# Kernel tuning notes

Measured on AMD Instinct MI355X. Metric: run time of the kernel, lower is better.

The kernel has to match this reference:

```python
import jax, jax.numpy as jnp
import numpy as np

N_NODES = 50000
N_EDGES = 800000
HIDDEN = 128
NUM_BASIS = 32
CUTOFF = 5.0


def setup_inputs() -> dict:
    key = jax.random.key(0)
    ks = jax.random.split(key, 9)
    node_features = jax.random.normal(ks[0], (N_NODES, HIDDEN), dtype=jnp.float32)
    positions = jax.random.normal(ks[1], (N_NODES, 3), dtype=jnp.float32)
    edge_index = jax.random.randint(ks[2], (2, N_EDGES), 0, N_NODES)
    edge_in = 2 * HIDDEN + NUM_BASIS
    W1 = jax.random.normal(ks[3], (edge_in, HIDDEN), dtype=jnp.float32) * (edge_in ** -0.5)
    b1 = jnp.zeros((HIDDEN,), dtype=jnp.float32)
    W2 = jax.random.normal(ks[4], (HIDDEN, HIDDEN), dtype=jnp.float32) * (HIDDEN ** -0.5)
    b2 = jnp.zeros((HIDDEN,), dtype=jnp.float32)
    Wo = jax.random.normal(ks[5], (HIDDEN, HIDDEN), dtype=jnp.float32) * (HIDDEN ** -0.5)
    bo = jnp.zeros((HIDDEN,), dtype=jnp.float32)
    return dict(node_features=node_features, positions=positions, edge_index=edge_index,
                W1=W1, b1=b1, W2=W2, b2=b2, Wo=Wo, bo=bo)


def reference(node_features, positions, edge_index, W1, b1, W2, b2, Wo, bo):
    n_nodes = node_features.shape[0]
    # Gaussian radial basis (fixed buffers)
    centers = jnp.linspace(0.0, CUTOFF, NUM_BASIS)  # [NB]
    width = 0.5 * (centers[1] - centers[0] + 0.01)
    src, dst = edge_index[0], edge_index[1]
    rel = positions[dst] - positions[src]                       # [E,3]
    dist = jnp.linalg.norm(rel, axis=-1)                        # [E]
    d = jnp.minimum(dist, CUTOFF)
    rbf = jnp.exp(-0.5 * ((d[:, None] - centers) / width) ** 2)  # [E,NB]
    # edge message: concat(src feats, dst feats, rbf) -> 2-layer SiLU MLP
    msg = jnp.concatenate([node_features[src], node_features[dst], rbf], axis=-1)  # [E,2H+NB]
    h = jax.nn.silu(msg @ W1 + b1) @ W2 + b2                    # [E,H]
    # scatter-add to destination nodes + degree normalization
    updates = jax.ops.segment_sum(h, dst, num_segments=n_nodes)          # [N,H]
    degree = jax.ops.segment_sum(jnp.ones_like(dist), dst, num_segments=n_nodes)
    updates = updates / jnp.maximum(degree, 1.0)[:, None]
    return updates @ Wo + bo
```

## Files before the change

kernel.cpp:

```cpp
#include <hip/hip_runtime.h>
#include <hip/hip_bf16.h>

#define NN 50000
#define NE 800000
#define HID 128
#define NB 32
#define SCAN_B 196

typedef short short8 __attribute__((ext_vector_type(8)));
typedef float f32x4 __attribute__((ext_vector_type(4)));

static __device__ __forceinline__ short f2bf(float x) {
    union { __hip_bfloat16 h; short s; } r;
    r.h = __float2bfloat16(x);
    return r.s;
}
static __device__ __forceinline__ float bf2f(unsigned short s) {
    return __uint_as_float(((unsigned int)s) << 16);
}
static __device__ __forceinline__ unsigned int addpack(unsigned int a, unsigned int b) {
    union { unsigned int u; __hip_bfloat162 h; } x, y, r;
    x.u = a; y.u = b;
    r.h = __hadd2(x.h, y.h);
    return r.u;
}

__global__ void fused_prep(const int* __restrict__ dstI, int* __restrict__ counts,
                           const float* __restrict__ W1, const float* __restrict__ W2,
                           const float* __restrict__ Wo,
                           short* __restrict__ W1aT, short* __restrict__ W1bT,
                           short* __restrict__ W1cT, short* __restrict__ W2t,
                           short* __restrict__ Wot) {
    int b = blockIdx.x;
    if (b < 3125) {
        int e = b * 256 + threadIdx.x;
        atomicAdd(&counts[dstI[e]], 1);
    } else {
        int t = (b - 3125) * 256 + threadIdx.x;
        if (t < 16384) {
            int n = t >> 7, k = t & 127;
            W1aT[t] = f2bf(W1[k * HID + n]);
        } else if ((t -= 16384) < 16384) {
            int n = t >> 7, k = t & 127;
            W1bT[t] = f2bf(W1[(k + 128) * HID + n]);
        } else if ((t -= 16384) < 4096) {
            int n = t >> 5, k = t & 31;
            W1cT[t] = f2bf(W1[(k + 256) * HID + n]);
        } else if ((t -= 4096) < 16384) {
            int n = t >> 7, k = t & 127;
            W2t[t] = f2bf(W2[k * HID + n]);
        } else if ((t -= 16384) < 16384) {
            int n = t >> 7, k = t & 127;
            Wot[t] = f2bf(Wo[k * HID + n]);
        }
    }
}

__global__ void k_scan1(const int* __restrict__ counts, int* __restrict__ scanEx,
                        int* __restrict__ blockSum) {
    __shared__ int s[256];
    int t = threadIdx.x, idx = blockIdx.x * 256 + t;
    int v = counts[idx];
    s[t] = v; __syncthreads();
    #pragma unroll
    for (int off = 1; off < 256; off <<= 1) {
        int x = (t >= off) ? s[t - off] : 0;
        __syncthreads();
        s[t] += x;
        __syncthreads();
    }
    scanEx[idx] = s[t] - v;
    if (t == 255) blockSum[blockIdx.x] = s[255];
}

__global__ void k_scan23(const int* __restrict__ scanEx, const int* __restrict__ blockSum,
                         int* __restrict__ cur) {
    __shared__ int s[256];
    int t = threadIdx.x, b = blockIdx.x;
    s[t] = (t < b) ? blockSum[t] : 0;
    __syncthreads();
    #pragma unroll
    for (int off = 128; off > 0; off >>= 1) {
        if (t < off) s[t] += s[t + off];
        __syncthreads();
    }
    int idx = b * 256 + t;
    cur[idx] = scanEx[idx] + s[0];
}

__global__ void k_permute(const int* __restrict__ src, const int* __restrict__ dst,
                          int* __restrict__ cur, int2* __restrict__ edgeS) {
    int e = blockIdx.x * 256 + threadIdx.x;
    int s = src[e];
    int d = dst[e];
    int r = atomicAdd(&cur[d], 1);
    edgeS[r] = make_int2(s, d);
}

__global__ void sd_kernel(const float* __restrict__ nf,
                          const short* __restrict__ W1aT, const short* __restrict__ W1bT,
                          short* __restrict__ Sg, short* __restrict__ Dg) {
    __shared__ short As[64 * 136];
    const int tid  = threadIdx.x;
    const int wave = tid >> 6;
    const int lane = tid & 63;
    const int quad = lane >> 4;
    const int l15  = lane & 15;
    const int n0   = blockIdx.x * 64;

    {
        int row = tid >> 2, pt = tid & 3;
        int node = min(n0 + row, NN - 1);
        const float4* p = (const float4*)(nf + (size_t)node * HID + pt * 32);
        #pragma unroll
        for (int j = 0; j < 4; ++j) {
            float4 w0 = p[j * 2], w1 = p[j * 2 + 1];
            short8 o;
            o[0] = f2bf(w0.x); o[1] = f2bf(w0.y); o[2] = f2bf(w0.z); o[3] = f2bf(w0.w);
            o[4] = f2bf(w1.x); o[5] = f2bf(w1.y); o[6] = f2bf(w1.z); o[7] = f2bf(w1.w);
            *(short8*)(As + row * 136 + pt * 32 + j * 8) = o;
        }
    }
    __syncthreads();

    f32x4 aS[4][2], aD[4][2];
    #pragma unroll
    for (int mt = 0; mt < 4; ++mt)
        #pragma unroll
        for (int nt = 0; nt < 2; ++nt) {
            aS[mt][nt] = (f32x4){0.f, 0.f, 0.f, 0.f};
            aD[mt][nt] = (f32x4){0.f, 0.f, 0.f, 0.f};
        }

    #pragma unroll
    for (int kk = 0; kk < 4; ++kk) {
        int ko = kk * 32 + quad * 8;
        short8 a[4];
        #pragma unroll
        for (int mt = 0; mt < 4; ++mt)
            a[mt] = *(const short8*)(As + (mt * 16 + l15) * 136 + ko);
        #pragma unroll
        for (int nt = 0; nt < 2; ++nt) {
            int n = wave * 32 + nt * 16 + l15;
            short8 bS = *(const short8*)(W1aT + n * HID + ko);
            short8 bD = *(const short8*)(W1bT + n * HID + ko);
            #pragma unroll
            for (int mt = 0; mt < 4; ++mt) {
                aS[mt][nt] = __builtin_amdgcn_mfma_f32_16x16x32_bf16(a[mt], bS, aS[mt][nt], 0, 0, 0);
                aD[mt][nt] = __builtin_amdgcn_mfma_f32_16x16x32_bf16(a[mt], bD, aD[mt][nt], 0, 0, 0);
            }
        }
    }

    #pragma unroll
    for (int nt = 0; nt < 2; ++nt) {
        int col = wave * 32 + nt * 16 + l15;
        #pragma unroll
        for (int mt = 0; mt < 4; ++mt) {
            #pragma unroll
            for (int r = 0; r < 4; ++r) {
                int node = n0 + mt * 16 + quad * 4 + r;
                if (node < NN) {
                    Sg[(size_t)node * HID + col] = f2bf(aS[mt][nt][r]);
                    Dg[(size_t)node * HID + col] = f2bf(aD[mt][nt][r]);
                }
            }
        }
    }
}

__launch_bounds__(512, 6)
__global__ void edge_kernel(const short* __restrict__ Sg,
                            const short* __restrict__ Dg,
                            const float* __restrict__ pos,
                            const int2* __restrict__ edgeS,
                            const short* __restrict__ W1cT,
                            const float* __restrict__ b1,
                            const short* __restrict__ W2t,
                            const float* __restrict__ b2,
                            float* __restrict__ upd) {
    __shared__ char buf[49152];
    __shared__ int  dn_sh[128];
    short* PRE = (short*)buf;
    short* R   = (short*)(buf + 34816);
    short* Ps  = (short*)buf;
    float* UfT = (float*)buf;

    const int tid  = threadIdx.x;
    const int wave = tid >> 6;
    const int lane = tid & 63;
    const int quad = lane >> 4;
    const int l15  = lane & 15;
    const int mg   = wave >> 2;
    const int nsl  = wave & 3;
    const int e0   = blockIdx.x * 128;

    {
        int es = tid >> 2, pt = tid & 3;
        int2 sd = edgeS[e0 + es];
        int s = sd.x, d = sd.y;
        const int4* sp = (const int4*)(Sg + (size_t)s * HID + pt * 32);
        const int4* dp = (const int4*)(Dg + (size_t)d * HID + pt * 32);
        int4* op = (int4*)(PRE + es * 136 + pt * 32);
        #pragma unroll
        for (int j = 0; j < 4; ++j) {
            int4 a = sp[j], b = dp[j];
            int4 o;
            o.x = addpack(a.x, b.x);
            o.y = addpack(a.y, b.y);
            o.z = addpack(a.z, b.z);
            o.w = addpack(a.w, b.w);
            op[j] = o;
        }
        if (pt == 0) dn_sh[es] = d;
        float dx = pos[d * 3 + 0] - pos[s * 3 + 0];
        float dy = pos[d * 3 + 1] - pos[s * 3 + 1];
        float dz = pos[d * 3 + 2] - pos[s * 3 + 2];
        float dd = fminf(sqrtf(dx * dx + dy * dy + dz * dz), 5.0f);
        const float step  = 5.0f / 31.0f;
        const float width = 0.5f * (step + 0.01f);
        const float coef  = -0.5f / (width * width);
        short8 r;
        #pragma unroll
        for (int j = 0; j < 8; ++j) {
            float c = step * (float)(pt * 8 + j);
            float t = dd - c;
            r[j] = f2bf(__expf(coef * t * t));
        }
        *(short8*)(R + es * 56 + pt * 8) = r;
    }
    __syncthreads();

    f32x4 acc[4][2];
    #pragma unroll
    for (int mt = 0; mt < 4; ++mt)
        #pragma unroll
        for (int nt = 0; nt < 2; ++nt) acc[mt][nt] = (f32x4){0.f, 0.f, 0.f, 0.f};
    {
        int ko = quad * 8;
        short8 a[4];
        #pragma unroll
        for (int mt = 0; mt < 4; ++mt)
            a[mt] = *(const short8*)(R + (mg * 64 + mt * 16 + l15) * 56 + ko);
        #pragma unroll
        for (int nt = 0; nt < 2; ++nt) {
            int n = nsl * 32 + nt * 16 + l15;
            short8 b = *(const short8*)(W1cT + n * NB + ko);
            #pragma unroll
            for (int mt = 0; mt < 4; ++mt)
                acc[mt][nt] = __builtin_amdgcn_mfma_f32_16x16x32_bf16(a[mt], b, acc[mt][nt], 0, 0, 0);
        }
    }

    {
        float b1c[2] = { b1[nsl * 32 + l15], b1[nsl * 32 + 16 + l15] };
        const unsigned short* PREu = (const unsigned short*)PRE;
        #pragma unroll
        for (int nt = 0; nt < 2; ++nt) {
            int col = nsl * 32 + nt * 16 + l15;
            #pragma unroll
            for (int mt = 0; mt < 4; ++mt) {
                #pragma unroll
                for (int r = 0; r < 4; ++r) {
                    int row = mg * 64 + mt * 16 + quad * 4 + r;
                    float pre = bf2f(PREu[row * 136 + col]);
                    float x = acc[mt][nt][r] + pre + b1c[nt];
                    float p = x * __builtin_amdgcn_rcpf(1.0f + __expf(-x));
                    Ps[row * 136 + col] = f2bf(p);
                }
            }
        }
    }
    __syncthreads();

    f32x4 acc2[4][2];
    #pragma unroll
    for (int mt = 0; mt < 4; ++mt)
        #pragma unroll
        for (int nt = 0; nt < 2; ++nt) acc2[mt][nt] = (f32x4){0.f, 0.f, 0.f, 0.f};

    #pragma unroll
    for (int kk = 0; kk < 4; ++kk) {
        int ko = kk * 32 + quad * 8;
        short8 a[4];
        #pragma unroll
        for (int mt = 0; mt < 4; ++mt)
            a[mt] = *(const short8*)(Ps + (mg * 64 + mt * 16 + l15) * 136 + ko);
        #pragma unroll
        for (int nt = 0; nt < 2; ++nt) {
            int n = nsl * 32 + nt * 16 + l15;
            short8 b = *(const short8*)(W2t + n * HID + ko);
            #pragma unroll
            for (int mt = 0; mt < 4; ++mt)
                acc2[mt][nt] = __builtin_amdgcn_mfma_f32_16x16x32_bf16(a[mt], b, acc2[mt][nt], 0, 0, 0);
        }
    }
    __syncthreads();

    float b2c[2] = { b2[nsl * 32 + l15], b2[nsl * 32 + 16 + l15] };
    #pragma unroll
    for (int h = 0; h < 2; ++h) {
        if (mg == h) {
            #pragma unroll
            for (int nt = 0; nt < 2; ++nt) {
                int col = nsl * 32 + nt * 16 + l15;
                #pragma unroll
                for (int mt = 0; mt < 4; ++mt) {
                    f32x4 v;
                    #pragma unroll
                    for (int r = 0; r < 4; ++r) v[r] = acc2[mt][nt][r] + b2c[nt];
                    *(f32x4*)(UfT + col * 68 + mt * 16 + quad * 4) = v;
                }
            }
        }
        __syncthreads();
        {
            int col = tid & 127;
            int seg = tid >> 7;
            int rb  = h * 64 + seg * 16;
            const float* cp = UfT + col * 68 + seg * 16;
            f32x4 vv[4];
            #pragma unroll
            for (int j = 0; j < 4; ++j) vv[j] = *(const f32x4*)(cp + j * 4);
            int rnode = dn_sh[rb];
            float run = 0.0f;
            #pragma unroll
            for (int i = 0; i < 16; ++i) {
                int node = dn_sh[rb + i];
                float v = vv[i >> 2][i & 3];
                if (node != rnode) {
                    atomicAdd(upd + (size_t)rnode * HID + col, run);
                    rnode = node;
                    run = v;
                } else {
                    run += v;
                }
            }
            atomicAdd(upd + (size_t)rnode * HID + col, run);
        }
        __syncthreads();
    }
}

__launch_bounds__(256, 4)
__global__ void out_kernel(float* __restrict__ out,
                           const int* __restrict__ counts,
                           const short* __restrict__ Wot,
                           const float* __restrict__ bo) {
    __shared__ short A2[64 * 136];

    const int tid  = threadIdx.x;
    const int wave = tid >> 6;
    const int lane = tid & 63;
    const int quad = lane >> 4;
    const int l15  = lane & 15;
    const int n0   = blockIdx.x * 64;

    {
        int row = tid >> 2, pt = tid & 3;
        int node = n0 + row;
        if (node < NN) {
            float inv = 1.0f / fmaxf((float)counts[node], 1.0f);
            const float4* p = (const float4*)(out + (size_t)node * HID + pt * 32);
            #pragma unroll
            for (int j = 0; j < 4; ++j) {
                float4 w0 = p[j * 2], w1 = p[j * 2 + 1];
                short8 o;
                o[0] = f2bf(w0.x * inv); o[1] = f2bf(w0.y * inv);
                o[2] = f2bf(w0.z * inv); o[3] = f2bf(w0.w * inv);
                o[4] = f2bf(w1.x * inv); o[5] = f2bf(w1.y * inv);
                o[6] = f2bf(w1.z * inv); o[7] = f2bf(w1.w * inv);
                *(short8*)(A2 + row * 136 + pt * 32 + j * 8) = o;
            }
        } else {
            short8 z = (short8){0, 0, 0, 0, 0, 0, 0, 0};
            #pragma unroll
            for (int j = 0; j < 4; ++j)
                *(short8*)(A2 + row * 136 + pt * 32 + j * 8) = z;
        }
    }
    __syncthreads();

    f32x4 acc[4][2];
    #pragma unroll
    for (int mt = 0; mt < 4; ++mt)
        #pragma unroll
        for (int nt = 0; nt < 2; ++nt) acc[mt][nt] = (f32x4){0.f, 0.f, 0.f, 0.f};

    #pragma unroll
    for (int kk = 0; kk < 4; ++kk) {
        int ko = kk * 32 + quad * 8;
        short8 a[4];
        #pragma unroll
        for (int mt = 0; mt < 4; ++mt)
            a[mt] = *(const short8*)(A2 + (mt * 16 + l15) * 136 + ko);
        #pragma unroll
        for (int nt = 0; nt < 2; ++nt) {
            int n = wave * 32 + nt * 16 + l15;
            short8 b = *(const short8*)(Wot + n * HID + ko);
            #pragma unroll
            for (int mt = 0; mt < 4; ++mt)
                acc[mt][nt] = __builtin_amdgcn_mfma_f32_16x16x32_bf16(a[mt], b, acc[mt][nt], 0, 0, 0);
        }
    }
    __syncthreads();

    #pragma unroll
    for (int nt = 0; nt < 2; ++nt) {
        int col = wave * 32 + nt * 16 + l15;
        float bias = bo[col];
        #pragma unroll
        for (int mt = 0; mt < 4; ++mt) {
            #pragma unroll
            for (int r = 0; r < 4; ++r) {
                int row = mt * 16 + quad * 4 + r;
                int node = n0 + row;
                if (node < NN)
                    out[(size_t)node * HID + col] = acc[mt][nt][r] + bias;
            }
        }
    }
}

extern "C" void kernel_launch(void* const* d_in, const int* in_sizes, int n_in,
                              void* d_out, int out_size, void* d_ws, size_t ws_size,
                              hipStream_t stream) {
    const float* nf  = (const float*)d_in[0];
    const float* pos = (const float*)d_in[1];
    const int*   ei  = (const int*)d_in[2];
    const float* W1  = (const float*)d_in[3];
    const float* b1  = (const float*)d_in[4];
    const float* W2  = (const float*)d_in[5];
    const float* b2  = (const float*)d_in[6];
    const float* Wo  = (const float*)d_in[7];
    const float* bo  = (const float*)d_in[8];
    float* out = (float*)d_out;

    char* ws = (char*)d_ws;
    short* W1aT     = (short*)(ws);
    short* W1bT     = (short*)(ws + 32768);
    short* W1cT     = (short*)(ws + 65536);
    short* W2t      = (short*)(ws + 73728);
    short* Wot      = (short*)(ws + 106496);
    int*   counts   = (int*)(ws + 139264);
    int*   cur      = (int*)(ws + 339968);
    int*   blockSum = (int*)(ws + 540672);
    int2*  edgeS    = (int2*)(ws + 541696);
    short* Sg       = (short*)(ws + 6941696);
    short* Dg       = (short*)(ws + 19741696);
    int*   scanEx   = (int*)Sg;

    (void)hipMemsetAsync(out, 0, (size_t)NN * HID * sizeof(float), stream);
    (void)hipMemsetAsync(counts, 0, 200704, stream);

    fused_prep<<<3397, 256, 0, stream>>>(ei + NE, counts, W1, W2, Wo,
                                         W1aT, W1bT, W1cT, W2t, Wot);
    k_scan1<<<SCAN_B, 256, 0, stream>>>(counts, scanEx, blockSum);
    k_scan23<<<SCAN_B, 256, 0, stream>>>(scanEx, blockSum, cur);
    k_permute<<<3125, 256, 0, stream>>>(ei, ei + NE, cur, edgeS);
    sd_kernel<<<(NN + 63) / 64, 256, 0, stream>>>(nf, W1aT, W1bT, Sg, Dg);
    edge_kernel<<<NE / 128, 512, 0, stream>>>(Sg, Dg, pos, edgeS,
                                              W1cT, b1, W2t, b2, out);
    out_kernel<<<(NN + 63) / 64, 256, 0, stream>>>(out, counts, Wot, bo);
}
```

Measured before the change: 327.1 us.

## Fuse permute into sd kernel, fold output zeroing into prep, stage stores via LDS

Merges the edge-permutation kernel and the node projection kernel into one launch, using extra blocks for the permutation work. It drops the separate memset of the output and zeroes it inside the prep kernel with a grid-stride loop. The S/D projection results are staged through shared memory so the global bf16 stores become coalesced 16-byte row writes instead of scattered 2-byte stores. This saves launches and store transactions, at the cost of extra barriers and a heavier prep kernel.

```diff
diff --git a/kernel.cpp b/kernel.cpp
--- a/kernel.cpp
+++ b/kernel.cpp
@@ -6,6 +6,7 @@
 #define HID 128
 #define NB 32
 #define SCAN_B 196
+#define SD_B 782
 
 typedef short short8 __attribute__((ext_vector_type(8)));
 typedef float f32x4 __attribute__((ext_vector_type(4)));
@@ -30,8 +31,16 @@
                            const float* __restrict__ Wo,
                            short* __restrict__ W1aT, short* __restrict__ W1bT,
                            short* __restrict__ W1cT, short* __restrict__ W2t,
-                           short* __restrict__ Wot) {
+                           short* __restrict__ Wot,
+                           float* __restrict__ out) {
     int b = blockIdx.x;
+    {
+        int gtid = b * 256 + threadIdx.x;
+        const int nthr = 3397 * 256;
+        float4 z = make_float4(0.f, 0.f, 0.f, 0.f);
+        for (int i = gtid; i < NN * HID / 4; i += nthr)
+            ((float4*)out)[i] = z;
+    }
     if (b < 3125) {
         int e = b * 256 + threadIdx.x;
         atomicAdd(&counts[dstI[e]], 1);
@@ -88,28 +97,32 @@
     cur[idx] = scanEx[idx] + s[0];
 }
 
-__global__ void k_permute(const int* __restrict__ src, const int* __restrict__ dst,
-                          int* __restrict__ cur, int2* __restrict__ edgeS) {
-    int e = blockIdx.x * 256 + threadIdx.x;
-    int s = src[e];
-    int d = dst[e];
-    int r = atomicAdd(&cur[d], 1);
-    edgeS[r] = make_int2(s, d);
-}
-
-__global__ void sd_kernel(const float* __restrict__ nf,
-                          const short* __restrict__ W1aT, const short* __restrict__ W1bT,
-                          short* __restrict__ Sg, short* __restrict__ Dg) {
+__launch_bounds__(256, 4)
+__global__ void perm_sd(const float* __restrict__ nf,
+                        const short* __restrict__ W1aT, const short* __restrict__ W1bT,
+                        short* __restrict__ Sg, short* __restrict__ Dg,
+                        const int* __restrict__ src, const int* __restrict__ dst,
+                        int* __restrict__ cur, int2* __restrict__ edgeS) {
     __shared__ short As[64 * 136];
-    const int tid  = threadIdx.x;
+    const int tid = threadIdx.x;
+
+    if (blockIdx.x >= SD_B) {
+        int e = (blockIdx.x - SD_B) * 256 + tid;
+        int s = src[e];
+        int d = dst[e];
+        int r = atomicAdd(&cur[d], 1);
+        edgeS[r] = make_int2(s, d);
+        return;
+    }
+
     const int wave = tid >> 6;
     const int lane = tid & 63;
     const int quad = lane >> 4;
     const int l15  = lane & 15;
     const int n0   = blockIdx.x * 64;
-
-    {
-        int row = tid >> 2, pt = tid & 3;
+    const int row  = tid >> 2, pt = tid & 3;
+
+    {
         int node = min(n0 + row, NN - 1);
         const float4* p = (const float4*)(nf + (size_t)node * HID + pt * 32);
         #pragma unroll
@@ -151,21 +164,41 @@
             }
         }
     }
+    __syncthreads();
 
     #pragma unroll
     for (int nt = 0; nt < 2; ++nt) {
         int col = wave * 32 + nt * 16 + l15;
         #pragma unroll
-        for (int mt = 0; mt < 4; ++mt) {
-            #pragma unroll
-            for (int r = 0; r < 4; ++r) {
-                int node = n0 + mt * 16 + quad * 4 + r;
-                if (node < NN) {
-                    Sg[(size_t)node * HID + col] = f2bf(aS[mt][nt][r]);
-                    Dg[(size_t)node * HID + col] = f2bf(aD[mt][nt][r]);
-                }
-            }
-        }
+        for (int mt = 0; mt < 4; ++mt)
+            #pragma unroll
+            for (int r = 0; r < 4; ++r)
+                As[(mt * 16 + quad * 4 + r) * 136 + col] = f2bf(aS[mt][nt][r]);
+    }
+    __syncthreads();
+    if (n0 + row < NN) {
+        short8* gp = (short8*)(Sg + (size_t)(n0 + row) * HID + pt * 32);
+        #pragma unroll
+        for (int j = 0; j < 4; ++j)
+            gp[j] = *(const short8*)(As + row * 136 + pt * 32 + j * 8);
+    }
+    __syncthreads();
+
+    #pragma unroll
+    for (int nt = 0; nt < 2; ++nt) {
+        int col = wave * 32 + nt * 16 + l15;
+        #pragma unroll
+        for (int mt = 0; mt < 4; ++mt)
+            #pragma unroll
+            for (int r = 0; r < 4; ++r)
+                As[(mt * 16 + quad * 4 + r) * 136 + col] = f2bf(aD[mt][nt][r]);
+    }
+    __syncthreads();
+    if (n0 + row < NN) {
+        short8* gp = (short8*)(Dg + (size_t)(n0 + row) * HID + pt * 32);
+        #pragma unroll
+        for (int j = 0; j < 4; ++j)
+            gp[j] = *(const short8*)(As + row * 136 + pt * 32 + j * 8);
     }
 }
 
@@ -450,15 +483,14 @@
     short* Dg       = (short*)(ws + 19741696);
     int*   scanEx   = (int*)Sg;
 
-    (void)hipMemsetAsync(out, 0, (size_t)NN * HID * sizeof(float), stream);
     (void)hipMemsetAsync(counts, 0, 200704, stream);
 
     fused_prep<<<3397, 256, 0, stream>>>(ei + NE, counts, W1, W2, Wo,
-                                         W1aT, W1bT, W1cT, W2t, Wot);
+                                         W1aT, W1bT, W1cT, W2t, Wot, out);
     k_scan1<<<SCAN_B, 256, 0, stream>>>(counts, scanEx, blockSum);
     k_scan23<<<SCAN_B, 256, 0, stream>>>(scanEx, blockSum, cur);
-    k_permute<<<3125, 256, 0, stream>>>(ei, ei + NE, cur, edgeS);
-    sd_kernel<<<(NN + 63) / 64, 256, 0, stream>>>(nf, W1aT, W1bT, Sg, Dg);
+    perm_sd<<<SD_B + 3125, 256, 0, stream>>>(nf, W1aT, W1bT, Sg, Dg,
+                                             ei, ei + NE, cur, edgeS);
     edge_kernel<<<NE / 128, 512, 0, stream>>>(Sg, Dg, pos, edgeS,
                                               W1cT, b1, W2t, b2, out);
     out_kernel<<<(NN + 63) / 64, 256, 0, stream>>>(out, counts, Wot, bo);
```

New measurement: 325.6 us, median of 2. Within noise of the previous version (-0.4%).
